# Kernel tuning notes

Hardware: AMD Instinct MI355X
Metric: run time of the kernel (lower is better)

Reference implementation:

```python
import jax, jax.numpy as jnp
import numpy as np

VOCAB = 4233
D = 256  # word_dim = hidden_size = proj_size


def lstm_cell(x, h, c, Wih, Whh, bih, bhh):
    # PyTorch LSTM gate order: i, f, g, o
    gates = x @ Wih.T + h @ Whh.T + bih + bhh
    i, f, g, o = jnp.split(gates, 4, axis=-1)
    c = jax.nn.sigmoid(f) * c + jax.nn.sigmoid(i) * jnp.tanh(g)
    h = jax.nn.sigmoid(o) * jnp.tanh(c)
    return h, c


def setup_inputs() -> dict:
    key = jax.random.key(0)
    ks = jax.random.split(key, 20)
    B, T, U = 64, 1024, 100
    inp = {
        'eout': jax.random.normal(ks[0], (B, T, D), dtype=jnp.float32),
        'x_mask': jnp.ones((B, T, 1), dtype=jnp.float32),
        'y': jax.random.randint(ks[1], (B, U), 0, VOCAB),
        'y_mask': jnp.ones((B, U), dtype=jnp.float32),
        'emb': jax.random.normal(ks[2], (VOCAB, D), dtype=jnp.float32) * 0.1,
        'w_w': jax.random.uniform(ks[3], (D, D), minval=-0.05, maxval=0.05),
        'w_b': jnp.zeros((D,), dtype=jnp.float32),
        'v_w': jax.random.uniform(ks[4], (D, D), minval=-0.05, maxval=0.05),
        'v_b': jnp.zeros((D,), dtype=jnp.float32),
        'w_att_v': jax.random.normal(ks[5], (D,), dtype=jnp.float32) * 0.02,
        'Wih_att': jax.random.normal(ks[6], (4 * D, 2 * D), dtype=jnp.float32) * 0.05,
        'Whh_att': jax.random.normal(ks[7], (4 * D, D), dtype=jnp.float32) * 0.05,
        'bih_att': jnp.zeros((4 * D,), dtype=jnp.float32),
        'bhh_att': jnp.zeros((4 * D,), dtype=jnp.float32),
        'Wih_dec': jax.random.normal(ks[8], (4 * D, 2 * D), dtype=jnp.float32) * 0.05,
        'Whh_dec': jax.random.normal(ks[9], (4 * D, D), dtype=jnp.float32) * 0.05,
        'bih_dec': jnp.zeros((4 * D,), dtype=jnp.float32),
        'bhh_dec': jnp.zeros((4 * D,), dtype=jnp.float32),
        'cls_w': jax.random.normal(ks[10], (VOCAB, 3 * D), dtype=jnp.float32) * 0.02,
        'cls_b': jnp.zeros((VOCAB,), dtype=jnp.float32),
    }
    return inp


def reference(eout, x_mask, y, y_mask, emb, w_w, w_b, v_w, v_b, w_att_v,
              Wih_att, Whh_att, bih_att, bhh_att,
              Wih_dec, Whh_dec, bih_dec, bhh_dec, cls_w, cls_b):
    B = eout.shape[0]
    att_h = eout @ w_w.T + w_b                      # [B, T, D]
    embed = emb[y[:, :-1]]                          # [B, U-1, D]
    mask_add = (x_mask[:, :, 0] - 1.0) * 1e30       # [B, T]
    zeros = jnp.zeros((B, D), dtype=eout.dtype)

    def att_step(carry, e_t):
        h, c, ctx = carry
        x_t = jnp.concatenate([e_t, ctx], axis=1)   # [B, 2D]
        h, c = lstm_cell(x_t, h, c, Wih_att, Whh_att, bih_att, bhh_att)
        state = h @ v_w.T + v_b                     # [B, D]
        scores = jnp.sum(w_att_v * jnp.tanh(state[:, None, :] + att_h), axis=2) + mask_add
        alpha = jax.nn.softmax(scores, axis=1)      # [B, T]
        ctx = jnp.einsum('bt,btd->bd', alpha, eout)
        return (h, c, ctx), (h, ctx)

    _, (hs, ctxs) = jax.lax.scan(att_step, (zeros, zeros, zeros), jnp.swapaxes(embed, 0, 1))
    ym = y_mask[:, 1:, None]
    lstms = jnp.swapaxes(hs, 0, 1) * ym             # [B, U-1, D]
    contexts = jnp.swapaxes(ctxs, 0, 1) * ym        # [B, U-1, D]
    att_fea = jnp.concatenate([lstms, contexts], axis=2)  # [B, U-1, 2D]

    def dec_step(carry, x_t):
        h, c = carry
        h, c = lstm_cell(x_t, h, c, Wih_dec, Whh_dec, bih_dec, bhh_dec)
        return (h, c), h

    _, dh = jax.lax.scan(dec_step, (zeros, zeros), jnp.swapaxes(att_fea, 0, 1))
    dout = jnp.concatenate([att_fea, jnp.swapaxes(dh, 0, 1)], axis=2)  # [B, U-1, 3D]
    # dropout is identity at eval
    dout = dout * ym
    logit = dout @ cls_w.T + cls_b                  # 1x1 conv2d == linear
    return logit
```

## Files before the change

### kernel.cpp

```cpp
#include <hip/hip_runtime.h>


typedef unsigned short u16;
typedef unsigned int u32;
typedef short bf16x8_t __attribute__((ext_vector_type(8)));
typedef float f32x4_t __attribute__((ext_vector_type(4)));

#define NBLK 256
#define LOG2E 1.4426950408889634f
#define FP32_PAT 0x3F800000u

__device__ __forceinline__ float bf2f(u16 h) {
  return __builtin_bit_cast(float, (u32)h << 16);
}
__device__ __forceinline__ u16 f2bf(float f) {
  u32 u = __builtin_bit_cast(u32, f);
  return (u16)((u + 0x7fffu + ((u >> 16) & 1u)) >> 16);
}
__device__ __forceinline__ void bf8_to_f32(uint4 v, float* o) {
  o[0] = __builtin_bit_cast(float, v.x << 16);
  o[1] = __builtin_bit_cast(float, v.x & 0xffff0000u);
  o[2] = __builtin_bit_cast(float, v.y << 16);
  o[3] = __builtin_bit_cast(float, v.y & 0xffff0000u);
  o[4] = __builtin_bit_cast(float, v.z << 16);
  o[5] = __builtin_bit_cast(float, v.z & 0xffff0000u);
  o[6] = __builtin_bit_cast(float, v.w << 16);
  o[7] = __builtin_bit_cast(float, v.w & 0xffff0000u);
}
__device__ __forceinline__ float sigm(float x) {
  float e = __builtin_amdgcn_exp2f(x * -LOG2E);
  return __builtin_amdgcn_rcpf(1.f + e);
}
__device__ __forceinline__ float tanh_(float x) {
  float e = __builtin_amdgcn_exp2f(x * (2.f * LOG2E));
  return 1.f - 2.f * __builtin_amdgcn_rcpf(e + 1.f);
}
__device__ __forceinline__ bool probe_f32(const void* xm) {
  return *(const u32*)xm == FP32_PAT;
}

__device__ __forceinline__ void gstore(float* p, float v) {
  __hip_atomic_store((u32*)p, __builtin_bit_cast(u32, v),
                     __ATOMIC_RELAXED, __HIP_MEMORY_SCOPE_AGENT);
}
__device__ __forceinline__ float gload(const float* p) {
  u32 u = __hip_atomic_load((const u32*)p, __ATOMIC_RELAXED,
                            __HIP_MEMORY_SCOPE_AGENT);
  return __builtin_bit_cast(float, u);
}

__device__ __forceinline__ void gbar2(u32* slots, u32 ep) {
  __syncthreads();
  if (threadIdx.x == 0)
    __hip_atomic_store(slots + (size_t)blockIdx.x * 32, ep,
                       __ATOMIC_RELAXED, __HIP_MEMORY_SCOPE_AGENT);
  if (threadIdx.x < 256) {
    const u32* s = slots + (size_t)threadIdx.x * 32;
    while (__hip_atomic_load(s, __ATOMIC_RELAXED, __HIP_MEMORY_SCOPE_AGENT) < ep)
      __builtin_amdgcn_s_sleep(2);
  }
  __syncthreads();
}

#define NSEG 18
struct Segs {
  const void* src[NSEG];
  u16* dst[NSEG];
  int n[NSEG];
};
__global__ void k_convert(Segs S, const u32* __restrict__ probe) {
  if (*probe != FP32_PAT) return;
  int seg = blockIdx.y;
  const float* src = (const float*)S.src[seg];
  u16* dst = S.dst[seg];
  int n = S.n[seg];
  for (int i = blockIdx.x * 256 + threadIdx.x; i < n; i += gridDim.x * 256)
    dst[i] = f2bf(src[i]);
}

__global__ void k_vwt(const void* __restrict__ v_w, u16* __restrict__ vwT,
                      const u32* __restrict__ probe) {
  bool f32 = (*probe == FP32_PAT);
  int idx = blockIdx.x * 256 + threadIdx.x;
  int k = idx >> 8, d = idx & 255;
  vwT[idx] = f32 ? f2bf(((const float*)v_w)[d * 256 + k])
                 : ((const u16*)v_w)[d * 256 + k];
}

__global__ __launch_bounds__(256) void k_atth(
    const void* __restrict__ eout_o, const u16* __restrict__ eoutB,
    const void* __restrict__ w_w_o, const u16* __restrict__ w_wB,
    const void* __restrict__ w_b_o, const u16* __restrict__ w_bB,
    u16* __restrict__ Ta, const u32* __restrict__ probe) {
  bool f32 = (*probe == FP32_PAT);
  const u16* eout = f32 ? eoutB : (const u16*)eout_o;
  const u16* w_w = f32 ? w_wB : (const u16*)w_w_o;
  const u16* w_b = f32 ? w_bB : (const u16*)w_b_o;
  int wave = threadIdx.x >> 6, lane = threadIdx.x & 63;
  int lm = lane & 15, lk8 = (lane >> 4) * 8;
  int m0 = blockIdx.x * 64 + wave * 16;
  int n0 = blockIdx.y * 64;
  f32x4_t acc[4] = {{0,0,0,0},{0,0,0,0},{0,0,0,0},{0,0,0,0}};
  const u16* arow = eout + (size_t)(m0 + lm) * 256 + lk8;
  for (int k0 = 0; k0 < 256; k0 += 32) {
    bf16x8_t af = *(const bf16x8_t*)(arow + k0);
#pragma unroll
    for (int nt = 0; nt < 4; ++nt) {
      const u16* brow = w_w + (size_t)(n0 + nt * 16 + lm) * 256 + k0 + lk8;
      bf16x8_t bf = *(const bf16x8_t*)brow;
      acc[nt] = __builtin_amdgcn_mfma_f32_16x16x32_bf16(af, bf, acc[nt], 0, 0, 0);
    }
  }
  int rb = (lane >> 4) * 4;
#pragma unroll
  for (int nt = 0; nt < 4; ++nt) {
    int n = n0 + nt * 16 + lm;
    float bias = bf2f(w_b[n]);
#pragma unroll
    for (int r2 = 0; r2 < 4; ++r2) {
      int m = m0 + rb + r2;
      Ta[(size_t)m * 256 + n] = f2bf(tanh_(acc[nt][r2] + bias));
    }
  }
}

__global__ __launch_bounds__(256) void k_logit(
    const u16* __restrict__ dout,
    const void* __restrict__ cls_w_o, const u16* __restrict__ cls_wB,
    const void* __restrict__ cls_b_o, const u16* __restrict__ cls_bB,
    void* __restrict__ outp, const u32* __restrict__ probe) {
  bool f32 = (*probe == FP32_PAT);
  const u16* cls_w = f32 ? cls_wB : (const u16*)cls_w_o;
  const u16* cls_b = f32 ? cls_bB : (const u16*)cls_b_o;
  int wave = threadIdx.x >> 6, lane = threadIdx.x & 63;
  int lm = lane & 15, lk8 = (lane >> 4) * 8;
  int m0 = blockIdx.x * 64 + wave * 16;
  int n0 = blockIdx.y * 64;
  f32x4_t acc[4] = {{0,0,0,0},{0,0,0,0},{0,0,0,0},{0,0,0,0}};
  const u16* arow = dout + (size_t)(m0 + lm) * 768 + lk8;
#pragma unroll 4
  for (int k0 = 0; k0 < 768; k0 += 32) {
    bf16x8_t af = *(const bf16x8_t*)(arow + k0);
#pragma unroll
    for (int nt = 0; nt < 4; ++nt) {
      int n = n0 + nt * 16 + lm;
      int bn = (n < 4233) ? n : 0;
      bf16x8_t bf = *(const bf16x8_t*)(cls_w + (size_t)bn * 768 + k0 + lk8);
      acc[nt] = __builtin_amdgcn_mfma_f32_16x16x32_bf16(af, bf, acc[nt], 0, 0, 0);
    }
  }
  int rb = (lane >> 4) * 4;
#pragma unroll
  for (int nt = 0; nt < 4; ++nt) {
    int n = n0 + nt * 16 + lm;
    if (n < 4233) {
      float bias = bf2f(cls_b[n]);
#pragma unroll
      for (int r2 = 0; r2 < 4; ++r2) {
        int m = m0 + rb + r2;
        float v = acc[nt][r2] + bias;
        if (f32) ((float*)outp)[(size_t)m * 4233 + n] = v;
        else     ((u16*)outp)[(size_t)m * 4233 + n] = f2bf(v);
      }
    }
  }
}

__device__ __forceinline__ void p1_gemm(
    const u16* __restrict__ Wih, const u16* __restrict__ Whh,
    const float (*x_l)[512], const float (*h_l)[256],
    float (*scr)[65], int tid, int hug) {
  int r = tid & 63, kq = tid >> 6;
  int hu = hug * 16 + (r >> 2), gate = r & 3;
  int wrow = gate * 256 + hu;
  float acc[8] = {0, 0, 0, 0, 0, 0, 0, 0};
  const u16* wp = Wih + (size_t)wrow * 512 + kq * 64;
#pragma unroll 4
  for (int c = 0; c < 8; ++c) {
    float wf[8];
    bf8_to_f32(*(const uint4*)(wp + c * 8), wf);
#pragma unroll
    for (int b = 0; b < 8; ++b) {
      const float* xp = &x_l[b][kq * 64 + c * 8];
#pragma unroll
      for (int j = 0; j < 8; ++j) acc[b] += wf[j] * xp[j];
    }
  }
  const u16* wp2 = Whh + (size_t)wrow * 256 + kq * 32;
#pragma unroll 4
  for (int c = 0; c < 4; ++c) {
    float wf[8];
    bf8_to_f32(*(const uint4*)(wp2 + c * 8), wf);
#pragma unroll
    for (int b = 0; b < 8; ++b) {
      const float* xp = &h_l[b][kq * 32 + c * 8];
#pragma unroll
      for (int j = 0; j < 8; ++j) acc[b] += wf[j] * xp[j];
    }
  }
#pragma unroll
  for (int b = 0; b < 8; ++b) scr[r][b * 8 + kq] = acc[b];
  __syncthreads();
}

__global__ __launch_bounds__(512) void k_scan(
    const void* __restrict__ eout_o, const u16* __restrict__ eoutB,
    const void* __restrict__ x_mask_o, const u16* __restrict__ x_maskB,
    const int* __restrict__ y,
    const void* __restrict__ y_mask_o, const u16* __restrict__ y_maskB,
    const void* __restrict__ emb_o, const u16* __restrict__ embB,
    const void* __restrict__ v_b_o, const u16* __restrict__ v_bB,
    const void* __restrict__ wav_o, const u16* __restrict__ wavB,
    const void* __restrict__ WihA_o, const u16* __restrict__ WihAB,
    const void* __restrict__ WhhA_o, const u16* __restrict__ WhhAB,
    const void* __restrict__ bihA_o, const u16* __restrict__ bihAB,
    const void* __restrict__ bhhA_o, const u16* __restrict__ bhhAB,
    const void* __restrict__ WihD_o, const u16* __restrict__ WihDB,
    const void* __restrict__ WhhD_o, const u16* __restrict__ WhhDB,
    const void* __restrict__ bihD_o, const u16* __restrict__ bihDB,
    const void* __restrict__ bhhD_o, const u16* __restrict__ bhhDB,
    u32* slots, float* h_dec, float* h_att,
    float* ctx_part, const u16* __restrict__ vwT, const u16* __restrict__ Ta,
    u16* __restrict__ dout) {
  __shared__ float x_l[8][512];
  __shared__ float h_l[8][256];
  __shared__ float scr[64][65];
  __shared__ float sp[512];
  __shared__ float hs_l[256], ts_l[256], wv_l[256], p_l[256];
  __shared__ float red_l[4];
  __shared__ float inv_es[8];
  __shared__ float ym_s[8];

  const bool f32 = probe_f32(x_mask_o);
  const u16* eout   = f32 ? eoutB  : (const u16*)eout_o;
  const u16* x_mask = f32 ? x_maskB: (const u16*)x_mask_o;
  const u16* y_mask = f32 ? y_maskB: (const u16*)y_mask_o;
  const u16* emb    = f32 ? embB   : (const u16*)emb_o;
  const u16* v_b    = f32 ? v_bB   : (const u16*)v_b_o;
  const u16* wav    = f32 ? wavB   : (const u16*)wav_o;
  const u16* WihA   = f32 ? WihAB  : (const u16*)WihA_o;
  const u16* WhhA   = f32 ? WhhAB  : (const u16*)WhhA_o;
  const u16* bihA   = f32 ? bihAB  : (const u16*)bihA_o;
  const u16* bhhA   = f32 ? bhhAB  : (const u16*)bhhA_o;
  const u16* WihD   = f32 ? WihDB  : (const u16*)WihD_o;
  const u16* WhhD   = f32 ? WhhDB  : (const u16*)WhhD_o;
  const u16* bihD   = f32 ? bihDB  : (const u16*)bihD_o;
  const u16* bhhD   = f32 ? bhhDB  : (const u16*)bhhD_o;

  const int tid = threadIdx.x, blk = blockIdx.x;
  const int bg = blk >> 5, sub = blk & 31;
  const bool is_att = (sub < 16);
  const int hug = is_att ? sub : (sub - 16);
  const int b2 = blk >> 2, tc = blk & 3;

  if (tid < 256) wv_l[tid] = bf2f(wav[tid]);
  float c_att_reg = 0.f;
  float c_dec_reg = 0.f;

  for (int t = 0; t <= 99; ++t) {
    if (is_att) {
      if (tid < 8 && t > 0) {
        const float* cp = ctx_part + (size_t)(bg * 8 + tid) * 4 * 257;
        float es = gload(cp + 256) + gload(cp + 257 + 256) +
                   gload(cp + 2 * 257 + 256) + gload(cp + 3 * 257 + 256);
        inv_es[tid] = 1.f / fmaxf(es, 1e-30f);
      }
      __syncthreads();
      for (int i = tid; i < 2048; i += 512) {
        int b = i >> 8, d = i & 255;
        int bglob = bg * 8 + b;
        int yv = y[bglob * 100 + t];
        x_l[b][d] = bf2f(emb[(size_t)yv * 256 + d]);
        float cx = 0.f;
        if (t > 0) {
          const float* cp = ctx_part + (size_t)bglob * 4 * 257;
          float s0 = gload(cp + d) + gload(cp + 257 + d) +
                     gload(cp + 2 * 257 + d) + gload(cp + 3 * 257 + d);
          cx = s0 * inv_es[b];
        }
        x_l[b][256 + d] = cx;
        h_l[b][d] = gload(h_att + (t & 1) * 16384 + bglob * 256 + d);
      }
      __syncthreads();
      if (t >= 1 && tid < 128) {
        int b = tid >> 4, dl = tid & 15;
        int bglob = bg * 8 + b, u = t - 1;
        float ym = bf2f(y_mask[bglob * 100 + u + 1]);
        float ym2 = ym * ym;
        int hu = hug * 16 + dl;
        size_t orow = ((size_t)bglob * 99 + u) * 768;
        dout[orow + hu] = f2bf(h_l[b][hu] * ym2);
        dout[orow + 256 + hu] = f2bf(x_l[b][256 + hu] * ym2);
      }
      if (t < 99) {
        p1_gemm(WihA, WhhA, x_l, h_l, scr, tid, hug);
        if (tid < 128) {
          int b = tid >> 4, dl = tid & 15;
          int bglob = bg * 8 + b;
          float g4[4];
#pragma unroll
          for (int gate = 0; gate < 4; ++gate) {
            int r2 = dl * 4 + gate;
            int wrow2 = gate * 256 + hug * 16 + dl;
            float sg = bf2f(bihA[wrow2]) + bf2f(bhhA[wrow2]);
#pragma unroll
            for (int q = 0; q < 8; ++q) sg += scr[r2][b * 8 + q];
            g4[gate] = sg;
          }
          float ii = sigm(g4[0]), ff = sigm(g4[1]), gg = tanh_(g4[2]), oo = sigm(g4[3]);
          float cn = ff * c_att_reg + ii * gg;
          c_att_reg = cn;
          float hn = oo * tanh_(cn);
          gstore(h_att + ((t + 1) & 1) * 16384 + bglob * 256 + hug * 16 + dl, hn);
        }
      }
    } else {
      if (t >= 1) {
        int s = t - 1;
        if (tid < 8) {
          int bglob = bg * 8 + tid;
          const float* cp = ctx_part + (size_t)bglob * 4 * 257;
          float es = gload(cp + 256) + gload(cp + 257 + 256) +
                     gload(cp + 2 * 257 + 256) + gload(cp + 3 * 257 + 256);
          inv_es[tid] = 1.f / fmaxf(es, 1e-30f);
          ym_s[tid] = bf2f(y_mask[bglob * 100 + s + 1]);
        }
        __syncthreads();
        for (int i = tid; i < 2048; i += 512) {
          int b = i >> 8, d = i & 255;
          int bglob = bg * 8 + b;
          float ym = ym_s[b];
          const float* cp = ctx_part + (size_t)bglob * 4 * 257;
          float s0 = gload(cp + d) + gload(cp + 257 + d) +
                     gload(cp + 2 * 257 + d) + gload(cp + 3 * 257 + d);
          float cx = s0 * inv_es[b];
          x_l[b][d] = gload(h_att + (t & 1) * 16384 + bglob * 256 + d) * ym;
          x_l[b][256 + d] = cx * ym;
          h_l[b][d] = gload(h_dec + (s & 1) * 16384 + bglob * 256 + d);
        }
        __syncthreads();
        p1_gemm(WihD, WhhD, x_l, h_l, scr, tid, hug);
        if (tid < 128) {
          int b = tid >> 4, dl = tid & 15;
          int bglob = bg * 8 + b;
          float g4[4];
#pragma unroll
          for (int gate = 0; gate < 4; ++gate) {
            int r2 = dl * 4 + gate;
            int wrow2 = gate * 256 + hug * 16 + dl;
            float sg = bf2f(bihD[wrow2]) + bf2f(bhhD[wrow2]);
#pragma unroll
            for (int q = 0; q < 8; ++q) sg += scr[r2][b * 8 + q];
            g4[gate] = sg;
          }
          float ii = sigm(g4[0]), ff = sigm(g4[1]), gg = tanh_(g4[2]), oo = sigm(g4[3]);
          float cn = ff * c_dec_reg + ii * gg;
          c_dec_reg = cn;
          float hn = oo * tanh_(cn);
          int hu_g = hug * 16 + dl;
          gstore(h_dec + ((s + 1) & 1) * 16384 + bglob * 256 + hu_g, hn);
          float ym = ym_s[b];
          dout[((size_t)bglob * 99 + s) * 768 + 512 + hu_g] = f2bf(hn * ym);
        }
      }
    }
    if (t == 99) break;
    gbar2(slots, (u32)(2 * t + 1));

    {
      int b = b2;
      if (tid < 256)
        hs_l[tid] = gload(h_att + ((t + 1) & 1) * 16384 + b * 256 + tid);
      __syncthreads();
      {
        int n = tid & 255, half = tid >> 8;
        const u16* col = vwT + (size_t)(half * 128) * 256 + n;
        float st = 0.f;
#pragma unroll 16
        for (int k = 0; k < 128; ++k)
          st += hs_l[half * 128 + k] * bf2f(col[(size_t)k * 256]);
        sp[tid] = st;
      }
      __syncthreads();
      if (tid < 256)
        ts_l[tid] = tanh_(sp[tid] + sp[tid + 256] + bf2f(v_b[tid]));
      __syncthreads();
      {
        int pos = tid & 255, half = tid >> 8;
        int tg = tc * 256 + pos;
        const u16* ar = Ta + ((size_t)(b * 1024 + tg)) * 256 + half * 128;
        float sacc = 0.f;
#pragma unroll 8
        for (int d8 = 0; d8 < 128; d8 += 8) {
          float af[8];
          bf8_to_f32(*(const uint4*)(ar + d8), af);
#pragma unroll
          for (int j = 0; j < 8; ++j) {
            int d = half * 128 + d8 + j;
            float tsv = ts_l[d], ta = af[j];
            float u = tsv + ta;
            float v = fmaf(tsv, ta, 1.f);
            sacc = fmaf(wv_l[d] * u, __builtin_amdgcn_rcpf(fmaxf(v, 1e-6f)), sacc);
          }
        }
        sp[tid] = sacc;
      }
      __syncthreads();
      if (tid < 256) {
        int tg = tc * 256 + tid;
        float s = sp[tid] + sp[tid + 256];
        s += (bf2f(x_mask[b * 1024 + tg]) - 1.f) * 1e30f;
        s = fminf(s, 80.f);
        float p = __builtin_amdgcn_exp2f(s * LOG2E);
        p_l[tid] = p;
        float wsum = p;
#pragma unroll
        for (int off = 32; off; off >>= 1) wsum += __shfl_down(wsum, off);
        if ((tid & 63) == 0) red_l[tid >> 6] = wsum;
      }
      __syncthreads();
      {
        int d = tid & 255, half = tid >> 8;
        const u16* er = eout + ((size_t)(b * 1024 + tc * 256 + half * 128)) * 256 + d;
        float a0 = 0.f;
#pragma unroll 16
        for (int tt = 0; tt < 128; ++tt)
          a0 += p_l[half * 128 + tt] * bf2f(er[(size_t)tt * 256]);
        sp[tid] = a0;
      }
      __syncthreads();
      if (tid < 256) {
        float* cslot = ctx_part + (size_t)(b * 4 + tc) * 257;
        gstore(cslot + tid, sp[tid] + sp[tid + 256]);
        if (tid == 0)
          gstore(cslot + 256, red_l[0] + red_l[1] + red_l[2] + red_l[3]);
      }
    }
    gbar2(slots, (u32)(2 * t + 2));
  }
}

extern "C" void kernel_launch(void* const* d_in, const int* in_sizes, int n_in,
                              void* d_out, int out_size, void* d_ws, size_t ws_size,
                              hipStream_t stream) {
  (void)in_sizes; (void)n_in; (void)out_size; (void)ws_size;
  const void* eout    = d_in[0];
  const void* x_mask  = d_in[1];
  const int*  y       = (const int*)d_in[2];
  const void* y_mask  = d_in[3];
  const void* emb     = d_in[4];
  const void* w_w     = d_in[5];
  const void* w_b     = d_in[6];
  const void* v_w     = d_in[7];
  const void* v_b     = d_in[8];
  const void* w_att_v = d_in[9];
  const void* Wih_att = d_in[10];
  const void* Whh_att = d_in[11];
  const void* bih_att = d_in[12];
  const void* bhh_att = d_in[13];
  const void* Wih_dec = d_in[14];
  const void* Whh_dec = d_in[15];
  const void* bih_dec = d_in[16];
  const void* bhh_dec = d_in[17];
  const void* cls_w   = d_in[18];
  const void* cls_b   = d_in[19];
  const u32* probe = (const u32*)x_mask;

  u16* TaB   = (u16*)d_out;
  u16* eoutB = TaB + 16777216;

  char* w = (char*)d_ws;
  u32*   slots    = (u32*)(w + 0);
  float* h_dec    = (float*)(w + 32768);
  float* h_att    = (float*)(w + 163840);
  const size_t ZB = 229376;
  float* ctx_part = (float*)(w + 491520);
  u16*   vwT      = (u16*)(w + 754688);
  u16*   dout     = (u16*)(w + 885760);
  u16*   embB     = (u16*)(w + 10617856);
  u16*   WihAB    = (u16*)(w + 12785152);
  u16*   WhhAB    = (u16*)(w + 13833728);
  u16*   WihDB    = (u16*)(w + 14358016);
  u16*   WhhDB    = (u16*)(w + 15406592);
  u16*   bihAB    = (u16*)(w + 15930880);
  u16*   bhhAB    = (u16*)(w + 15932928);
  u16*   bihDB    = (u16*)(w + 15934976);
  u16*   bhhDB    = (u16*)(w + 15937024);
  u16*   v_bB     = (u16*)(w + 15939072);
  u16*   wavB     = (u16*)(w + 15939584);
  u16*   w_wB     = (u16*)(w + 15940096);
  u16*   w_bB     = (u16*)(w + 16071168);
  u16*   x_maskB  = (u16*)(w + 16071680);
  u16*   y_maskB  = (u16*)(w + 16202752);
  u16*   cls_wB   = (u16*)(w + 16215552);
  u16*   cls_bB   = (u16*)(w + 22717440);

  Segs S;
  const void* srcs[NSEG] = {eout, emb, Wih_att, Whh_att, Wih_dec, Whh_dec,
                            bih_att, bhh_att, bih_dec, bhh_dec, v_b, w_att_v,
                            w_w, w_b, x_mask, y_mask, cls_w, cls_b};
  u16* dsts[NSEG] = {eoutB, embB, WihAB, WhhAB, WihDB, WhhDB,
                     bihAB, bhhAB, bihDB, bhhDB, v_bB, wavB,
                     w_wB, w_bB, x_maskB, y_maskB, cls_wB, cls_bB};
  int ns[NSEG] = {16777216, 1083648, 524288, 262144, 524288, 262144,
                  1024, 1024, 1024, 1024, 256, 256,
                  65536, 256, 65536, 6400, 3250944, 4233};
  for (int i = 0; i < NSEG; ++i) { S.src[i] = srcs[i]; S.dst[i] = dsts[i]; S.n[i] = ns[i]; }

  hipMemsetAsync(d_ws, 0, ZB, stream);
  hipLaunchKernelGGL(k_convert, dim3(4096, NSEG), dim3(256), 0, stream, S, probe);
  hipLaunchKernelGGL(k_vwt, dim3(256), dim3(256), 0, stream, v_w, vwT, probe);
  hipLaunchKernelGGL(k_atth, dim3(1024, 4), dim3(256), 0, stream,
                     eout, eoutB, w_w, w_wB, w_b, w_bB, TaB, probe);
  hipLaunchKernelGGL(k_scan, dim3(NBLK), dim3(512), 0, stream,
                     eout, eoutB, x_mask, x_maskB, y, y_mask, y_maskB,
                     emb, embB, v_b, v_bB, w_att_v, wavB,
                     Wih_att, WihAB, Whh_att, WhhAB, bih_att, bihAB, bhh_att, bhhAB,
                     Wih_dec, WihDB, Whh_dec, WhhDB, bih_dec, bihDB, bhh_dec, bhhDB,
                     slots, h_dec, h_att, ctx_part, vwT, TaB, dout);
  hipLaunchKernelGGL(k_logit, dim3(99, 67), dim3(256), 0, stream,
                     dout, cls_w, cls_wB, cls_b, cls_bB, d_out, probe);
}
```

Measured before the change: 3.714 ms.

## Keep per-block att_h and eout tiles resident in registers across scan steps

```diff
diff --git a/kernel.cpp b/kernel.cpp
--- a/kernel.cpp
+++ b/kernel.cpp
@@ -62,7 +62,7 @@
   __syncthreads();
 }
 
-#define NSEG 18
+#define NSEG 19
 struct Segs {
   const void* src[NSEG];
   u16* dst[NSEG];
@@ -76,15 +76,6 @@
   int n = S.n[seg];
   for (int i = blockIdx.x * 256 + threadIdx.x; i < n; i += gridDim.x * 256)
     dst[i] = f2bf(src[i]);
-}
-
-__global__ void k_vwt(const void* __restrict__ v_w, u16* __restrict__ vwT,
-                      const u32* __restrict__ probe) {
-  bool f32 = (*probe == FP32_PAT);
-  int idx = blockIdx.x * 256 + threadIdx.x;
-  int k = idx >> 8, d = idx & 255;
-  vwT[idx] = f32 ? f2bf(((const float*)v_w)[d * 256 + k])
-                 : ((const u16*)v_w)[d * 256 + k];
 }
 
 __global__ __launch_bounds__(256) void k_atth(
@@ -203,13 +194,14 @@
   __syncthreads();
 }
 
-__global__ __launch_bounds__(512) void k_scan(
+__global__ __launch_bounds__(512, 2) void k_scan(
     const void* __restrict__ eout_o, const u16* __restrict__ eoutB,
     const void* __restrict__ x_mask_o, const u16* __restrict__ x_maskB,
     const int* __restrict__ y,
     const void* __restrict__ y_mask_o, const u16* __restrict__ y_maskB,
     const void* __restrict__ emb_o, const u16* __restrict__ embB,
     const void* __restrict__ v_b_o, const u16* __restrict__ v_bB,
+    const void* __restrict__ v_w_o, const u16* __restrict__ v_wB,
     const void* __restrict__ wav_o, const u16* __restrict__ wavB,
     const void* __restrict__ WihA_o, const u16* __restrict__ WihAB,
     const void* __restrict__ WhhA_o, const u16* __restrict__ WhhAB,
@@ -220,7 +212,7 @@
     const void* __restrict__ bihD_o, const u16* __restrict__ bihDB,
     const void* __restrict__ bhhD_o, const u16* __restrict__ bhhDB,
     u32* slots, float* h_dec, float* h_att,
-    float* ctx_part, const u16* __restrict__ vwT, const u16* __restrict__ Ta,
+    float* ctx_part, const u16* __restrict__ Ta,
     u16* __restrict__ dout) {
   __shared__ float x_l[8][512];
   __shared__ float h_l[8][256];
@@ -237,6 +229,7 @@
   const u16* y_mask = f32 ? y_maskB: (const u16*)y_mask_o;
   const u16* emb    = f32 ? embB   : (const u16*)emb_o;
   const u16* v_b    = f32 ? v_bB   : (const u16*)v_b_o;
+  const u16* v_w    = f32 ? v_wB   : (const u16*)v_w_o;
   const u16* wav    = f32 ? wavB   : (const u16*)wav_o;
   const u16* WihA   = f32 ? WihAB  : (const u16*)WihA_o;
   const u16* WhhA   = f32 ? WhhAB  : (const u16*)WhhA_o;
@@ -252,10 +245,30 @@
   const bool is_att = (sub < 16);
   const int hug = is_att ? sub : (sub - 16);
   const int b2 = blk >> 2, tc = blk & 3;
+  const int pos = tid & 255, half = tid >> 8;
 
   if (tid < 256) wv_l[tid] = bf2f(wav[tid]);
   float c_att_reg = 0.f;
   float c_dec_reg = 0.f;
+
+  uint4 ta_r[16];
+  {
+    const u16* ar = Ta + ((size_t)(b2 * 1024 + tc * 256 + pos)) * 256 + half * 128;
+#pragma unroll
+    for (int i = 0; i < 16; ++i) ta_r[i] = ((const uint4*)ar)[i];
+  }
+  u32 er_r[64];
+  {
+    const u16* er = eout + ((size_t)(b2 * 1024 + tc * 256 + half * 128)) * 256 + pos;
+#pragma unroll 8
+    for (int k = 0; k < 64; ++k) {
+      u32 lo = er[(size_t)(2 * k) * 256];
+      u32 hi = er[(size_t)(2 * k + 1) * 256];
+      er_r[k] = lo | (hi << 16);
+    }
+  }
+  const float xm_r = (bf2f(x_mask[b2 * 1024 + tc * 256 + pos]) - 1.f) * 1e30f;
+  const float vb_r = bf2f(v_b[pos]);
 
   for (int t = 0; t <= 99; ++t) {
     if (is_att) {
@@ -373,30 +386,30 @@
         hs_l[tid] = gload(h_att + ((t + 1) & 1) * 16384 + b * 256 + tid);
       __syncthreads();
       {
-        int n = tid & 255, half = tid >> 8;
-        const u16* col = vwT + (size_t)(half * 128) * 256 + n;
+        const u16* row = v_w + (size_t)pos * 256 + half * 128;
         float st = 0.f;
-#pragma unroll 16
-        for (int k = 0; k < 128; ++k)
-          st += hs_l[half * 128 + k] * bf2f(col[(size_t)k * 256]);
+#pragma unroll
+        for (int i = 0; i < 16; ++i) {
+          float wf[8];
+          bf8_to_f32(((const uint4*)row)[i], wf);
+#pragma unroll
+          for (int j = 0; j < 8; ++j) st += wf[j] * hs_l[half * 128 + i * 8 + j];
+        }
         sp[tid] = st;
       }
       __syncthreads();
       if (tid < 256)
-        ts_l[tid] = tanh_(sp[tid] + sp[tid + 256] + bf2f(v_b[tid]));
+        ts_l[tid] = tanh_(sp[tid] + sp[tid + 256] + vb_r);
       __syncthreads();
       {
-        int pos = tid & 255, half = tid >> 8;
-        int tg = tc * 256 + pos;
-        const u16* ar = Ta + ((size_t)(b * 1024 + tg)) * 256 + half * 128;
         float sacc = 0.f;
-#pragma unroll 8
-        for (int d8 = 0; d8 < 128; d8 += 8) {
+#pragma unroll
+        for (int i = 0; i < 16; ++i) {
           float af[8];
-          bf8_to_f32(*(const uint4*)(ar + d8), af);
+          bf8_to_f32(ta_r[i], af);
 #pragma unroll
           for (int j = 0; j < 8; ++j) {
-            int d = half * 128 + d8 + j;
+            int d = half * 128 + i * 8 + j;
             float tsv = ts_l[d], ta = af[j];
             float u = tsv + ta;
             float v = fmaf(tsv, ta, 1.f);
@@ -407,9 +420,7 @@
       }
       __syncthreads();
       if (tid < 256) {
-        int tg = tc * 256 + tid;
-        float s = sp[tid] + sp[tid + 256];
-        s += (bf2f(x_mask[b * 1024 + tg]) - 1.f) * 1e30f;
+        float s = sp[tid] + sp[tid + 256] + xm_r;
         s = fminf(s, 80.f);
         float p = __builtin_amdgcn_exp2f(s * LOG2E);
         p_l[tid] = p;
@@ -420,12 +431,15 @@
       }
       __syncthreads();
       {
-        int d = tid & 255, half = tid >> 8;
-        const u16* er = eout + ((size_t)(b * 1024 + tc * 256 + half * 128)) * 256 + d;
         float a0 = 0.f;
-#pragma unroll 16
-        for (int tt = 0; tt < 128; ++tt)
-          a0 += p_l[half * 128 + tt] * bf2f(er[(size_t)tt * 256]);
+#pragma unroll
+        for (int k = 0; k < 64; ++k) {
+          u32 v = er_r[k];
+          a0 = fmaf(p_l[half * 128 + 2 * k],
+                    __builtin_bit_cast(float, v << 16), a0);
+          a0 = fmaf(p_l[half * 128 + 2 * k + 1],
+                    __builtin_bit_cast(float, v & 0xffff0000u), a0);
+        }
         sp[tid] = a0;
       }
       __syncthreads();
@@ -475,7 +489,7 @@
   float* h_att    = (float*)(w + 163840);
   const size_t ZB = 229376;
   float* ctx_part = (float*)(w + 491520);
-  u16*   vwT      = (u16*)(w + 754688);
+  u16*   v_wB     = (u16*)(w + 754688);
   u16*   dout     = (u16*)(w + 885760);
   u16*   embB     = (u16*)(w + 10617856);
   u16*   WihAB    = (u16*)(w + 12785152);
@@ -498,26 +512,25 @@
   Segs S;
   const void* srcs[NSEG] = {eout, emb, Wih_att, Whh_att, Wih_dec, Whh_dec,
                             bih_att, bhh_att, bih_dec, bhh_dec, v_b, w_att_v,
-                            w_w, w_b, x_mask, y_mask, cls_w, cls_b};
+                            w_w, w_b, x_mask, y_mask, cls_w, cls_b, v_w};
   u16* dsts[NSEG] = {eoutB, embB, WihAB, WhhAB, WihDB, WhhDB,
                      bihAB, bhhAB, bihDB, bhhDB, v_bB, wavB,
-                     w_wB, w_bB, x_maskB, y_maskB, cls_wB, cls_bB};
+                     w_wB, w_bB, x_maskB, y_maskB, cls_wB, cls_bB, v_wB};
   int ns[NSEG] = {16777216, 1083648, 524288, 262144, 524288, 262144,
                   1024, 1024, 1024, 1024, 256, 256,
-                  65536, 256, 65536, 6400, 3250944, 4233};
+                  65536, 256, 65536, 6400, 3250944, 4233, 65536};
   for (int i = 0; i < NSEG; ++i) { S.src[i] = srcs[i]; S.dst[i] = dsts[i]; S.n[i] = ns[i]; }
 
   hipMemsetAsync(d_ws, 0, ZB, stream);
   hipLaunchKernelGGL(k_convert, dim3(4096, NSEG), dim3(256), 0, stream, S, probe);
-  hipLaunchKernelGGL(k_vwt, dim3(256), dim3(256), 0, stream, v_w, vwT, probe);
   hipLaunchKernelGGL(k_atth, dim3(1024, 4), dim3(256), 0, stream,
                      eout, eoutB, w_w, w_wB, w_b, w_bB, TaB, probe);
   hipLaunchKernelGGL(k_scan, dim3(NBLK), dim3(512), 0, stream,
                      eout, eoutB, x_mask, x_maskB, y, y_mask, y_maskB,
-                     emb, embB, v_b, v_bB, w_att_v, wavB,
+                     emb, embB, v_b, v_bB, v_w, v_wB, w_att_v, wavB,
                      Wih_att, WihAB, Whh_att, WhhAB, bih_att, bihAB, bhh_att, bhhAB,
                      Wih_dec, WihDB, Whh_dec, WhhDB, bih_dec, bihDB, bhh_dec, bhhDB,
-                     slots, h_dec, h_att, ctx_part, vwT, TaB, dout);
+                     slots, h_dec, h_att, ctx_part, TaB, dout);
   hipLaunchKernelGGL(k_logit, dim3(99, 67), dim3(256), 0, stream,
                      dout, cls_w, cls_wB, cls_b, cls_bB, d_out, probe);
 }
```

Measured after the change: 6.788 ms. +82.8%, slower.

## Cache per-block eout tile in LDS and shrink scratch by aliasing shared buffers

Applied to the files above, without the earlier changes.

```diff
diff --git a/kernel.cpp b/kernel.cpp
--- a/kernel.cpp
+++ b/kernel.cpp
@@ -169,7 +169,7 @@
 __device__ __forceinline__ void p1_gemm(
     const u16* __restrict__ Wih, const u16* __restrict__ Whh,
     const float (*x_l)[512], const float (*h_l)[256],
-    float (*scr)[65], int tid, int hug) {
+    float* scr, int tid, int hug) {
   int r = tid & 63, kq = tid >> 6;
   int hu = hug * 16 + (r >> 2), gate = r & 3;
   int wrow = gate * 256 + hu;
@@ -198,8 +198,20 @@
       for (int j = 0; j < 8; ++j) acc[b] += wf[j] * xp[j];
     }
   }
-#pragma unroll
-  for (int b = 0; b < 8; ++b) scr[r][b * 8 + kq] = acc[b];
+  int slot = kq & 3;
+  if (kq < 4) {
+#pragma unroll
+    for (int b = 0; b < 8; ++b)
+      scr[r * 32 + ((b * 4 + slot + r) & 31)] = acc[b];
+  }
+  __syncthreads();
+  if (kq >= 4) {
+#pragma unroll
+    for (int b = 0; b < 8; ++b) {
+      int idx = r * 32 + ((b * 4 + slot + r) & 31);
+      scr[idx] += acc[b];
+    }
+  }
   __syncthreads();
 }
 
@@ -222,14 +234,18 @@
     u32* slots, float* h_dec, float* h_att,
     float* ctx_part, const u16* __restrict__ vwT, const u16* __restrict__ Ta,
     u16* __restrict__ dout) {
+  __shared__ u16 eout_l[65536];
   __shared__ float x_l[8][512];
   __shared__ float h_l[8][256];
-  __shared__ float scr[64][65];
-  __shared__ float sp[512];
-  __shared__ float hs_l[256], ts_l[256], wv_l[256], p_l[256];
-  __shared__ float red_l[4];
-  __shared__ float inv_es[8];
-  __shared__ float ym_s[8];
+  __shared__ float scr[2048];
+  float* sp     = (float*)x_l;
+  float* hs_l   = (float*)x_l + 512;
+  float* ts_l   = (float*)x_l + 768;
+  float* p_l    = (float*)x_l + 1024;
+  float* wv_l   = (float*)x_l + 1280;
+  float* red_l  = (float*)x_l + 1536;
+  float* inv_es = scr;
+  float* ym_s   = scr + 8;
 
   const bool f32 = probe_f32(x_mask_o);
   const u16* eout   = f32 ? eoutB  : (const u16*)eout_o;
@@ -252,10 +268,21 @@
   const bool is_att = (sub < 16);
   const int hug = is_att ? sub : (sub - 16);
   const int b2 = blk >> 2, tc = blk & 3;
-
-  if (tid < 256) wv_l[tid] = bf2f(wav[tid]);
+  const int pos = tid & 255, half = tid >> 8;
+
   float c_att_reg = 0.f;
   float c_dec_reg = 0.f;
+
+  const float xm_r = (bf2f(x_mask[b2 * 1024 + tc * 256 + pos]) - 1.f) * 1e30f;
+  const float vb_r = bf2f(v_b[pos]);
+
+  {
+    const u16* src = eout + (size_t)(b2 * 1024 + tc * 256) * 256;
+#pragma unroll
+    for (int k = 0; k < 16; ++k)
+      ((uint4*)eout_l)[k * 512 + tid] = ((const uint4*)src)[k * 512 + tid];
+  }
+  __syncthreads();
 
   for (int t = 0; t <= 99; ++t) {
     if (is_att) {
@@ -304,7 +331,8 @@
             int wrow2 = gate * 256 + hug * 16 + dl;
             float sg = bf2f(bihA[wrow2]) + bf2f(bhhA[wrow2]);
 #pragma unroll
-            for (int q = 0; q < 8; ++q) sg += scr[r2][b * 8 + q];
+            for (int q = 0; q < 4; ++q)
+              sg += scr[r2 * 32 + ((b * 4 + q + r2) & 31)];
             g4[gate] = sg;
           }
           float ii = sigm(g4[0]), ff = sigm(g4[1]), gg = tanh_(g4[2]), oo = sigm(g4[3]);
@@ -350,7 +378,8 @@
             int wrow2 = gate * 256 + hug * 16 + dl;
             float sg = bf2f(bihD[wrow2]) + bf2f(bhhD[wrow2]);
 #pragma unroll
-            for (int q = 0; q < 8; ++q) sg += scr[r2][b * 8 + q];
+            for (int q = 0; q < 4; ++q)
+              sg += scr[r2 * 32 + ((b * 4 + q + r2) & 31)];
             g4[gate] = sg;
           }
           float ii = sigm(g4[0]), ff = sigm(g4[1]), gg = tanh_(g4[2]), oo = sigm(g4[3]);
@@ -359,7 +388,7 @@
           float hn = oo * tanh_(cn);
           int hu_g = hug * 16 + dl;
           gstore(h_dec + ((s + 1) & 1) * 16384 + bglob * 256 + hu_g, hn);
-          float ym = ym_s[b];
+          float ym = bf2f(y_mask[bglob * 100 + s + 1]);
           dout[((size_t)bglob * 99 + s) * 768 + 512 + hu_g] = f2bf(hn * ym);
         }
       }
@@ -369,12 +398,13 @@
 
     {
       int b = b2;
-      if (tid < 256)
+      if (tid < 256) {
         hs_l[tid] = gload(h_att + ((t + 1) & 1) * 16384 + b * 256 + tid);
+        wv_l[tid] = bf2f(wav[tid]);
+      }
       __syncthreads();
       {
-        int n = tid & 255, half = tid >> 8;
-        const u16* col = vwT + (size_t)(half * 128) * 256 + n;
+        const u16* col = vwT + (size_t)(half * 128) * 256 + pos;
         float st = 0.f;
 #pragma unroll 16
         for (int k = 0; k < 128; ++k)
@@ -383,10 +413,9 @@
       }
       __syncthreads();
       if (tid < 256)
-        ts_l[tid] = tanh_(sp[tid] + sp[tid + 256] + bf2f(v_b[tid]));
+        ts_l[tid] = tanh_(sp[tid] + sp[tid + 256] + vb_r);
       __syncthreads();
       {
-        int pos = tid & 255, half = tid >> 8;
         int tg = tc * 256 + pos;
         const u16* ar = Ta + ((size_t)(b * 1024 + tg)) * 256 + half * 128;
         float sacc = 0.f;
@@ -407,9 +436,7 @@
       }
       __syncthreads();
       if (tid < 256) {
-        int tg = tc * 256 + tid;
-        float s = sp[tid] + sp[tid + 256];
-        s += (bf2f(x_mask[b * 1024 + tg]) - 1.f) * 1e30f;
+        float s = sp[tid] + sp[tid + 256] + xm_r;
         s = fminf(s, 80.f);
         float p = __builtin_amdgcn_exp2f(s * LOG2E);
         p_l[tid] = p;
@@ -420,12 +447,11 @@
       }
       __syncthreads();
       {
-        int d = tid & 255, half = tid >> 8;
-        const u16* er = eout + ((size_t)(b * 1024 + tc * 256 + half * 128)) * 256 + d;
+        const u16* erow = eout_l + (size_t)(half * 128) * 256 + pos;
         float a0 = 0.f;
 #pragma unroll 16
         for (int tt = 0; tt < 128; ++tt)
-          a0 += p_l[half * 128 + tt] * bf2f(er[(size_t)tt * 256]);
+          a0 += p_l[half * 128 + tt] * bf2f(erow[tt * 256]);
         sp[tid] = a0;
       }
       __syncthreads();
```

New measurement: 3.213 ms. 1.16x faster.
